# Kernel tuning notes

Measured on AMD Instinct MI355X. Metric: run time of the kernel, lower is better.

The kernel has to match this reference:

```python
import jax, jax.numpy as jnp
import numpy as np

B, C, HEADS, DH = 2, 1280, 20, 64
INNER = HEADS * DH
HW = 64
S = HW * HW
L = 77
ENC = 4096
GROUPS = 32
EPS = 1e-5
CREG = 1.0     # creg_ in __init__
NOATTN = 1.0   # global noattn
NORES = 1.0    # global noresidual


def setup_inputs() -> dict:
    key = jax.random.key(0)
    ks = jax.random.split(key, 10)
    std = 0.02
    return {
        "x": jax.random.normal(ks[0], (B, C, HW, HW), jnp.float32),
        "text": jax.random.normal(ks[1], (B, L, ENC), jnp.float32),
        "gn_gamma": jnp.ones((C,), jnp.float32),
        "gn_beta": jnp.zeros((C,), jnp.float32),
        "ln_gamma": jnp.ones((ENC,), jnp.float32),
        "ln_beta": jnp.zeros((ENC,), jnp.float32),
        "Wq": jax.random.normal(ks[2], (C, INNER), jnp.float32) * std,
        "bq": jnp.zeros((INNER,), jnp.float32),
        "Wk": jax.random.normal(ks[3], (ENC, INNER), jnp.float32) * std,
        "bk": jnp.zeros((INNER,), jnp.float32),
        "Wv": jax.random.normal(ks[4], (ENC, INNER), jnp.float32) * std,
        "bv": jnp.zeros((INNER,), jnp.float32),
        "Wo": jax.random.normal(ks[5], (INNER, C), jnp.float32) * std,
        "bo": jnp.zeros((C,), jnp.float32),
        "size_reg": jax.random.uniform(ks[6], (1, S, L), jnp.float32),
        "treg": jax.random.uniform(ks[7], (1,), jnp.float32),
        "mask": jax.random.randint(ks[8], (1, S, L), 0, 2, jnp.int32),
    }


def _group_norm(h, gamma, beta):
    # h: [B, C, S]; GroupNorm over (C//GROUPS, S) per group
    hg = h.reshape(B, GROUPS, -1)
    mu = hg.mean(-1, keepdims=True)
    var = hg.var(-1, keepdims=True)
    hn = ((hg - mu) * jax.lax.rsqrt(var + EPS)).reshape(B, C, S)
    return hn * gamma[None, :, None] + beta[None, :, None]


def _layer_norm(t, gamma, beta):
    mu = t.mean(-1, keepdims=True)
    var = t.var(-1, keepdims=True)
    return (t - mu) * jax.lax.rsqrt(var + EPS) * gamma + beta


def reference(x, text, gn_gamma, gn_beta, ln_gamma, ln_beta, Wq, bq, Wk, bk,
              Wv, bv, Wo, bo, size_reg, treg, mask):
    residual = x                              # [B, C, HW, HW]
    h = x.reshape(B, C, S)                    # spatial tokens
    h = _group_norm(h, gn_gamma, gn_beta).transpose(0, 2, 1)   # [B, S, C]
    enc = _layer_norm(text, ln_gamma, ln_beta)                  # [B, L, ENC]

    # head_to_batch_dim (out_dim=3): [B, T, inner] -> [B*heads, T, dh]
    q = (h @ Wq + bq).reshape(B, S, HEADS, DH).transpose(0, 2, 1, 3).reshape(B * HEADS, S, DH)
    k = (enc @ Wk + bk).reshape(B, L, HEADS, DH).transpose(0, 2, 1, 3).reshape(B * HEADS, L, DH)
    v = (enc @ Wv + bv).reshape(B, L, HEADS, DH).transpose(0, 2, 1, 3).reshape(B * HEADS, L, DH)

    scale = DH ** -0.5
    sim = jnp.einsum('bsd,bld->bsl', q, k) * scale            # [B*H, S, L]

    # region regularization applied only to the conditional (second) half
    half = (B * HEADS) // 2
    sim_u, sim_c = sim[:half], sim[half:]
    mn = sim_c.min(-1, keepdims=True)
    mx = sim_c.max(-1, keepdims=True)
    m = mask > 0                                               # [1, S, L] broadcasts over heads
    w = size_reg * CREG * treg[0]
    sim_c = sim_c + jnp.where(m, w, 0.0) * (mx - sim_c) - jnp.where(m, 0.0, w) * (sim_c - mn)
    sim = jnp.concatenate([sim_u, sim_c], axis=0)

    probs = jax.nn.softmax(sim, axis=-1)
    out = jnp.einsum('bsl,bld->bsd', probs, v)                 # [B*H, S, DH]
    # batch_to_head_dim: [B*H, S, DH] -> [B, S, inner]
    out = out.reshape(B, HEADS, S, DH).transpose(0, 2, 1, 3).reshape(B, S, INNER)
    out = out @ Wo + bo                                        # to_out[0]; dropout p=0
    out = out.transpose(0, 2, 1).reshape(residual.shape)       # [B, C, HW, HW]
    return out * NOATTN + residual * NORES
```

## Files before the change

### kernel.cpp

```cpp
#include <hip/hip_runtime.h>

typedef __bf16 bf16_t;
typedef __bf16 bf16x8 __attribute__((ext_vector_type(8)));
typedef float  f32x4  __attribute__((ext_vector_type(4)));
typedef unsigned int u32x4 __attribute__((ext_vector_type(4)));


__global__ __launch_bounds__(256) void k_transpose_cvt4(
    const float* __restrict__ w0, const float* __restrict__ w1,
    const float* __restrict__ w2, const float* __restrict__ w3,
    bf16_t* __restrict__ o0, bf16_t* __restrict__ o1,
    bf16_t* __restrict__ o2, bf16_t* __restrict__ o3)
{
  const int z = blockIdx.z;
  const float* in  = (z == 0) ? w0 : (z == 1) ? w1 : (z == 2) ? w2 : w3;
  bf16_t*      out = (z == 0) ? o0 : (z == 1) ? o1 : (z == 2) ? o2 : o3;
  const int R = (z < 2) ? 1280 : 4096;
  const int r0 = blockIdx.y * 64;
  if (r0 >= R) return;
  __shared__ float tile[64][33];
  const int c0 = blockIdx.x * 32;
  const int t = threadIdx.x;
#pragma unroll
  for (int it = 0; it < 8; ++it) {
    int r = it * 8 + (t >> 5), c = t & 31;
    tile[r][c] = in[(size_t)(r0 + r) * 1280 + c0 + c];
  }
  __syncthreads();
  {
    const int oc  = t >> 3;
    const int seg = t & 7;
    bf16x8 o;
#pragma unroll
    for (int e = 0; e < 8; ++e) o[e] = (bf16_t)tile[seg * 8 + e][oc];
    *(bf16x8*)(out + (size_t)(c0 + oc) * R + r0 + seg * 8) = o;
  }
}

__global__ __launch_bounds__(256) void k_gn_partial(
    const float* __restrict__ x, float* __restrict__ partial)
{
  const int bg    = blockIdx.x >> 5;
  const int chunk = blockIdx.x & 31;
  const float* p  = x + (size_t)bg * 163840 + (size_t)chunk * 5120;
  float s1 = 0.f, s2 = 0.f;
#pragma unroll
  for (int it = 0; it < 5; ++it) {
    float4 v = *(const float4*)(p + (size_t)(it * 256 + threadIdx.x) * 4);
    s1 += v.x + v.y + v.z + v.w;
    s2 += v.x * v.x + v.y * v.y + v.z * v.z + v.w * v.w;
  }
#pragma unroll
  for (int off = 32; off > 0; off >>= 1) {
    s1 += __shfl_down(s1, off);
    s2 += __shfl_down(s2, off);
  }
  __shared__ float r1[4], r2[4];
  if ((threadIdx.x & 63) == 0) { r1[threadIdx.x >> 6] = s1; r2[threadIdx.x >> 6] = s2; }
  __syncthreads();
  if (threadIdx.x == 0) {
    partial[blockIdx.x * 2]     = r1[0] + r1[1] + r1[2] + r1[3];
    partial[blockIdx.x * 2 + 1] = r2[0] + r2[1] + r2[2] + r2[3];
  }
}

__global__ __launch_bounds__(64) void k_gn_finalize(
    const float* __restrict__ partial, float* __restrict__ stats)
{
  const int bg = threadIdx.x;
  float t1 = 0.f, t2 = 0.f;
#pragma unroll
  for (int c = 0; c < 32; ++c) {
    t1 += partial[(bg * 32 + c) * 2];
    t2 += partial[(bg * 32 + c) * 2 + 1];
  }
  const float invN = 1.0f / 163840.0f;
  float mu  = t1 * invN;
  float var = t2 * invN - mu * mu;
  stats[bg * 2]     = mu;
  stats[bg * 2 + 1] = rsqrtf(var + 1e-5f);
}

__global__ __launch_bounds__(256) void k_gn_apply(
    const float* __restrict__ x, const float* __restrict__ stats,
    const float* __restrict__ gamma, const float* __restrict__ beta,
    bf16_t* __restrict__ h)
{
  __shared__ float tile[64][65];
  const int s0 = blockIdx.x * 64;
  const int c0 = blockIdx.y * 64;
  const int b  = blockIdx.z;
  const int t  = threadIdx.x;
#pragma unroll
  for (int it = 0; it < 16; ++it) {
    int cl = it * 4 + (t >> 6);
    int sl = t & 63;
    tile[cl][sl] = x[((size_t)(b * 1280 + c0 + cl) << 12) + s0 + sl];
  }
  __syncthreads();
#pragma unroll
  for (int it = 0; it < 2; ++it) {
    int i  = it * 256 + t;
    int sl = i >> 3;
    int cg = i & 7;
    bf16x8 o;
#pragma unroll
    for (int e = 0; e < 8; ++e) {
      int c  = c0 + cg * 8 + e;
      int g  = c / 40;
      float mu = stats[(b * 32 + g) * 2];
      float rs = stats[(b * 32 + g) * 2 + 1];
      o[e] = (bf16_t)((tile[cg * 8 + e][sl] - mu) * rs * gamma[c] + beta[c]);
    }
    *(bf16x8*)(h + (size_t)(b * 4096 + s0 + sl) * 1280 + c0 + cg * 8) = o;
  }
}

__global__ __launch_bounds__(256) void k_ln(
    const float* __restrict__ text, const float* __restrict__ g,
    const float* __restrict__ bta, bf16_t* __restrict__ enc)
{
  const int row = blockIdx.x;
  const float* p = text + (size_t)row * 4096;
  float s1 = 0.f, s2 = 0.f;
  for (int i = threadIdx.x; i < 1024; i += 256) {
    float4 v = *(const float4*)(p + (size_t)i * 4);
    s1 += v.x + v.y + v.z + v.w;
    s2 += v.x * v.x + v.y * v.y + v.z * v.z + v.w * v.w;
  }
#pragma unroll
  for (int off = 32; off > 0; off >>= 1) {
    s1 += __shfl_down(s1, off);
    s2 += __shfl_down(s2, off);
  }
  __shared__ float r1[4], r2[4], sh[2];
  if ((threadIdx.x & 63) == 0) { r1[threadIdx.x >> 6] = s1; r2[threadIdx.x >> 6] = s2; }
  __syncthreads();
  if (threadIdx.x == 0) {
    float t1 = r1[0] + r1[1] + r1[2] + r1[3];
    float t2 = r2[0] + r2[1] + r2[2] + r2[3];
    const float invN = 1.0f / 4096.0f;
    float mu  = t1 * invN;
    float var = t2 * invN - mu * mu;
    sh[0] = mu;
    sh[1] = rsqrtf(var + 1e-5f);
  }
  __syncthreads();
  const float mu = sh[0], rs = sh[1];
  for (int i = threadIdx.x; i < 1024; i += 256) {
    float4 v  = *(const float4*)(p + (size_t)i * 4);
    float4 gg = *(const float4*)(g + (size_t)i * 4);
    float4 bb = *(const float4*)(bta + (size_t)i * 4);
    bf16_t* o = enc + (size_t)row * 4096 + (size_t)i * 4;
    o[0] = (bf16_t)((v.x - mu) * rs * gg.x + bb.x);
    o[1] = (bf16_t)((v.y - mu) * rs * gg.y + bb.y);
    o[2] = (bf16_t)((v.z - mu) * rs * gg.z + bb.z);
    o[3] = (bf16_t)((v.w - mu) * rs * gg.w + bb.w);
  }
}

template <int EPI>
__global__ __launch_bounds__(256, 2) void k_gemm_big(
    const bf16_t* __restrict__ A, const bf16_t* __restrict__ BT,
    const float* __restrict__ bias, bf16_t* __restrict__ outb,
    const float* __restrict__ xres, float* __restrict__ dout,
    int lda, int klen, int nnt)
{
  __shared__ alignas(16) bf16_t smem[40960];
  const int tid  = threadIdx.x;
  const int lane = tid & 63;
  const int wv   = tid >> 6;

  const int cpx  = gridDim.x >> 3;
  const int nbid = (blockIdx.x & 7) * cpx + (blockIdx.x >> 3);
  const int mt   = nbid / nnt, ntile = nbid % nnt;
  const int m0   = mt * 256;
  const int n0   = ntile * 64;

  f32x4 acc[4][4];
  const f32x4 fz = {0.f, 0.f, 0.f, 0.f};
#pragma unroll
  for (int i = 0; i < 4; ++i)
#pragma unroll
    for (int j = 0; j < 4; ++j) acc[i][j] = fz;

  auto stage = [&](int buf, int kt) {
    bf16_t* sA = smem + buf * 16384;
    bf16_t* sB = smem + 32768 + buf * 4096;
#pragma unroll
    for (int it = 0; it < 8; ++it) {
      int slot = it * 256 + tid;
      int row  = slot >> 3, ch = slot & 7;
      const bf16_t* ga = A + (size_t)(m0 + row) * lda + kt + ((ch ^ (row & 7)) << 3);
      __builtin_amdgcn_global_load_lds(
          (const __attribute__((address_space(1))) void*)ga,
          (__attribute__((address_space(3))) void*)((char*)sA + slot * 16),
          16, 0, 0);
    }
#pragma unroll
    for (int it = 0; it < 2; ++it) {
      int slot = it * 256 + tid;
      int row  = slot >> 3, ch = slot & 7;
      const bf16_t* gb = BT + (size_t)(n0 + row) * lda + kt + ((ch ^ (row & 7)) << 3);
      __builtin_amdgcn_global_load_lds(
          (const __attribute__((address_space(1))) void*)gb,
          (__attribute__((address_space(3))) void*)((char*)sB + slot * 16),
          16, 0, 0);
    }
  };

  const int nt_k = klen >> 6;
  stage(0, 0);
  if (nt_k > 1) stage(1, 64);

  for (int t = 0; t < nt_k; ++t) {
    if (t + 1 < nt_k) { asm volatile("s_waitcnt vmcnt(10)" ::: "memory"); }
    else              { asm volatile("s_waitcnt vmcnt(0)" ::: "memory"); }
    __builtin_amdgcn_s_barrier();
    const char* pA = (const char*)(smem + (t & 1) * 16384);
    const char* pB = (const char*)(smem + 32768 + (t & 1) * 4096);
#pragma unroll
    for (int ks = 0; ks < 2; ++ks) {
      const int kb = ks * 64 + ((lane >> 4) << 4);
      bf16x8 af[4], bfg[4];
#pragma unroll
      for (int i = 0; i < 4; ++i) {
        int r = wv * 64 + i * 16 + (lane & 15);
        af[i] = *(const bf16x8*)(pA + r * 128 + (kb ^ ((r & 7) << 4)));
      }
#pragma unroll
      for (int j = 0; j < 4; ++j) {
        int c = j * 16 + (lane & 15);
        bfg[j] = *(const bf16x8*)(pB + c * 128 + (kb ^ ((c & 7) << 4)));
      }
#pragma unroll
      for (int i = 0; i < 4; ++i)
#pragma unroll
        for (int j = 0; j < 4; ++j)
          acc[i][j] = __builtin_amdgcn_mfma_f32_16x16x32_bf16(af[i], bfg[j], acc[i][j], 0, 0, 0);
    }
    asm volatile("s_waitcnt lgkmcnt(0)" ::: "memory");
    __builtin_amdgcn_s_barrier();
    if (t + 2 < nt_k) stage(t & 1, (t + 2) * 64);
  }

  if (EPI == 0) {
    bf16_t* cst = smem;
#pragma unroll
    for (int j = 0; j < 4; ++j) {
      const int n  = n0 + j * 16 + (lane & 15);
      const float bs = bias[n];
      const int cl = j * 16 + (lane & 15);
#pragma unroll
      for (int i = 0; i < 4; ++i) {
        const int rl = wv * 64 + i * 16 + ((lane >> 4) << 2);
#pragma unroll
        for (int r = 0; r < 4; ++r)
          cst[(rl + r) * 76 + cl] = (bf16_t)(acc[i][j][r] + bs);
      }
    }
    __syncthreads();
#pragma unroll
    for (int it = 0; it < 8; ++it) {
      int slot = it * 256 + tid;
      int row = slot >> 3, ch = slot & 7;
      u32x4 d = *(const u32x4*)(cst + row * 76 + ch * 8);
      *(u32x4*)(outb + (size_t)(m0 + row) * 1280 + n0 + ch * 8) = d;
    }
  } else {
#pragma unroll
    for (int i = 0; i < 4; ++i) {
      const int mrow = m0 + wv * 64 + i * 16 + ((lane >> 4) << 2);
#pragma unroll
      for (int j = 0; j < 4; ++j) {
        const int n = n0 + j * 16 + (lane & 15);
        const int b = mrow >> 12, s = mrow & 4095;
        const size_t off = ((size_t)(b * 1280 + n) << 12) + s;
        const float bs = bias[n];
        const float4 xr = *(const float4*)(xres + off);
        float4 o;
        o.x = acc[i][j][0] + bs + xr.x;
        o.y = acc[i][j][1] + bs + xr.y;
        o.z = acc[i][j][2] + bs + xr.z;
        o.w = acc[i][j][3] + bs + xr.w;
        *(float4*)(dout + off) = o;
      }
    }
  }
}

__global__ __launch_bounds__(256, 3) void k_gemm_kv(
    const bf16_t* __restrict__ A, const bf16_t* __restrict__ BT,
    float* __restrict__ outf, int M, int lda, int klen, int nnt, int nst)
{
  __shared__ alignas(16) bf16_t smem[24576];
  const int tid  = threadIdx.x;
  const int lane = tid & 63;
  const int wv   = tid >> 6;
  const int wm   = wv >> 1, wn = wv & 1;

  const int cpx  = gridDim.x >> 3;
  const int nbid = (blockIdx.x & 7) * cpx + (blockIdx.x >> 3);
  const int mt   = nbid / nnt, ntile = nbid % nnt;
  const int m0   = mt * 128;
  const int n0   = ntile * 64;
  const int kbeg = blockIdx.z * klen;

  f32x4 acc[4][2];
  const f32x4 fz = {0.f, 0.f, 0.f, 0.f};
#pragma unroll
  for (int i = 0; i < 4; ++i)
#pragma unroll
    for (int j = 0; j < 2; ++j) acc[i][j] = fz;

  auto stage = [&](int buf, int kt) {
    bf16_t* sA = smem + buf * 8192;
    bf16_t* sB = smem + 16384 + buf * 4096;
#pragma unroll
    for (int it = 0; it < 4; ++it) {
      int slot = it * 256 + tid;
      int row  = slot >> 3, ch = slot & 7;
      int grow = m0 + row; if (grow > M - 1) grow = M - 1;
      const bf16_t* ga = A + (size_t)grow * lda + kt + ((ch ^ (row & 7)) << 3);
      __builtin_amdgcn_global_load_lds(
          (const __attribute__((address_space(1))) void*)ga,
          (__attribute__((address_space(3))) void*)((char*)sA + slot * 16),
          16, 0, 0);
    }
#pragma unroll
    for (int it = 0; it < 2; ++it) {
      int slot = it * 256 + tid;
      int row  = slot >> 3, ch = slot & 7;
      const bf16_t* gb = BT + (size_t)(n0 + row) * lda + kt + ((ch ^ (row & 7)) << 3);
      __builtin_amdgcn_global_load_lds(
          (const __attribute__((address_space(1))) void*)gb,
          (__attribute__((address_space(3))) void*)((char*)sB + slot * 16),
          16, 0, 0);
    }
  };

  const int nt_k = klen >> 6;
  stage(0, kbeg);
  if (nt_k > 1) stage(1, kbeg + 64);

  for (int t = 0; t < nt_k; ++t) {
    if (t + 1 < nt_k) { asm volatile("s_waitcnt vmcnt(6)" ::: "memory"); }
    else              { asm volatile("s_waitcnt vmcnt(0)" ::: "memory"); }
    __builtin_amdgcn_s_barrier();
    const char* pA = (const char*)(smem + (t & 1) * 8192);
    const char* pB = (const char*)(smem + 16384 + (t & 1) * 4096);
#pragma unroll
    for (int ks = 0; ks < 2; ++ks) {
      const int kb = ks * 64 + ((lane >> 4) << 4);
      bf16x8 af[4], bfg[2];
#pragma unroll
      for (int i = 0; i < 4; ++i) {
        int r = wm * 64 + i * 16 + (lane & 15);
        af[i] = *(const bf16x8*)(pA + r * 128 + (kb ^ ((r & 7) << 4)));
      }
#pragma unroll
      for (int j = 0; j < 2; ++j) {
        int c = wn * 32 + j * 16 + (lane & 15);
        bfg[j] = *(const bf16x8*)(pB + c * 128 + (kb ^ ((c & 7) << 4)));
      }
#pragma unroll
      for (int i = 0; i < 4; ++i)
#pragma unroll
        for (int j = 0; j < 2; ++j)
          acc[i][j] = __builtin_amdgcn_mfma_f32_16x16x32_bf16(af[i], bfg[j], acc[i][j], 0, 0, 0);
    }
    asm volatile("s_waitcnt lgkmcnt(0)" ::: "memory");
    __builtin_amdgcn_s_barrier();
    if (t + 2 < nt_k) stage(t & 1, kbeg + (t + 2) * 64);
  }

#pragma unroll
  for (int i = 0; i < 4; ++i) {
    const int mrow = m0 + wm * 64 + i * 16 + ((lane >> 4) << 2);
#pragma unroll
    for (int j = 0; j < 2; ++j) {
      const int n = n0 + wn * 32 + j * 16 + (lane & 15);
#pragma unroll
      for (int r = 0; r < 4; ++r)
        if (mrow + r < M)
          outf[(size_t)blockIdx.z * 154 * nst + (size_t)(mrow + r) * nst + n] = acc[i][j][r];
    }
  }
}

__global__ __launch_bounds__(256) void k_kv_reduce(
    const float* __restrict__ part, const float* __restrict__ bk,
    const float* __restrict__ bv, bf16_t* __restrict__ kb, bf16_t* __restrict__ vb)
{
  const int idx = blockIdx.x * 256 + threadIdx.x;
  if (idx >= 154 * 2560) return;
  const int r = idx / 2560, n = idx % 2560;
  float s = (n < 1280) ? bk[n] : bv[n - 1280];
#pragma unroll
  for (int sp = 0; sp < 8; ++sp) s += part[(size_t)sp * (154 * 2560) + idx];
  if (n < 1280) kb[(size_t)r * 1280 + n] = (bf16_t)s;
  else          vb[(size_t)r * 1280 + n - 1280] = (bf16_t)s;
}

__global__ __launch_bounds__(256) void k_attn(
    const bf16_t* __restrict__ q, const bf16_t* __restrict__ kbuf,
    const bf16_t* __restrict__ vbuf, bf16_t* __restrict__ ao,
    const float* __restrict__ size_reg, const int* __restrict__ mask,
    const float* __restrict__ treg)
{
  __shared__ alignas(16) bf16_t sQ[64 * 64];
  __shared__ alignas(16) bf16_t sK[80 * 64];
  __shared__ alignas(16) bf16_t sVT[64 * 104];
  __shared__ alignas(16) bf16_t sP[4 * 16 * 104];
  const int s0   = blockIdx.x * 64;
  const int bh   = blockIdx.y;
  const int b    = bh / 20, head = bh % 20;
  const int tid  = threadIdx.x, lane = tid & 63, wv = tid >> 6;
  const int ntok = lane & 15;

  const u32x4 uz = {0u, 0u, 0u, 0u};
  for (int i = tid; i < 832; i += 256) ((u32x4*)sVT)[i] = uz;
  for (int i = tid; i < 832; i += 256) ((u32x4*)sP)[i]  = uz;

  const size_t qbase = ((size_t)(b * 4096 + s0)) * 1280 + head * 64;
  for (int slot = tid; slot < 512; slot += 256) {
    int row = slot >> 3, ch = slot & 7;
    u32x4 d = *(const u32x4*)(q + qbase + (size_t)row * 1280 + ((ch ^ (row & 7)) << 3));
    *(u32x4*)((char*)sQ + slot * 16) = d;
  }
  const size_t kvbase = ((size_t)(b * 77)) * 1280 + head * 64;
  for (int slot = tid; slot < 640; slot += 256) {
    int tok = slot >> 3, ch = slot & 7;
    u32x4 d = uz;
    if (tok < 77)
      d = *(const u32x4*)(kbuf + kvbase + (size_t)tok * 1280 + ((ch ^ (tok & 7)) << 3));
    *(u32x4*)((char*)sK + slot * 16) = d;
  }
  __syncthreads();
  for (int e = tid; e < 77 * 64; e += 256) {
    int tok = e >> 6, dh = e & 63;
    sVT[dh * 104 + tok] = vbuf[kvbase + (size_t)tok * 1280 + dh];
  }
  __syncthreads();

  f32x4 sim[5];
  const f32x4 fz = {0.f, 0.f, 0.f, 0.f};
#pragma unroll
  for (int nf = 0; nf < 5; ++nf) sim[nf] = fz;
  const int qrow = wv * 16 + (lane & 15);
#pragma unroll
  for (int ks = 0; ks < 2; ++ks) {
    const int kb = ks * 64 + ((lane >> 4) << 4);
    bf16x8 aq = *(const bf16x8*)((const char*)sQ + qrow * 128 + (kb ^ ((qrow & 7) << 4)));
#pragma unroll
    for (int nf = 0; nf < 5; ++nf) {
      int tok = nf * 16 + ntok;
      bf16x8 bk = *(const bf16x8*)((const char*)sK + tok * 128 + (kb ^ ((tok & 7) << 4)));
      sim[nf] = __builtin_amdgcn_mfma_f32_16x16x32_bf16(aq, bk, sim[nf], 0, 0, 0);
    }
  }

  float vv[5][4];
#pragma unroll
  for (int nf = 0; nf < 5; ++nf)
#pragma unroll
    for (int r = 0; r < 4; ++r) vv[nf][r] = sim[nf][r] * 0.125f;

  const int rbase = s0 + wv * 16 + ((lane >> 4) << 2);

  if (b == 1) {
    const float tr = treg[0];
#pragma unroll
    for (int r = 0; r < 4; ++r) {
      float mx = -1e30f, mn = 1e30f;
#pragma unroll
      for (int nf = 0; nf < 5; ++nf)
        if (nf * 16 + ntok < 77) { mx = fmaxf(mx, vv[nf][r]); mn = fminf(mn, vv[nf][r]); }
#pragma unroll
      for (int m = 1; m < 16; m <<= 1) {
        mx = fmaxf(mx, __shfl_xor(mx, m));
        mn = fminf(mn, __shfl_xor(mn, m));
      }
      const int srow = rbase + r;
#pragma unroll
      for (int nf = 0; nf < 5; ++nf) {
        int l = nf * 16 + ntok;
        if (l < 77) {
          float w  = size_reg[srow * 77 + l] * tr;
          int   mk = mask[srow * 77 + l];
          float v  = vv[nf][r];
          vv[nf][r] = (mk > 0) ? v + w * (mx - v) : v - w * (v - mn);
        }
      }
    }
  }

#pragma unroll
  for (int r = 0; r < 4; ++r) {
    float mx = -1e30f;
#pragma unroll
    for (int nf = 0; nf < 5; ++nf)
      if (nf * 16 + ntok < 77) mx = fmaxf(mx, vv[nf][r]);
#pragma unroll
    for (int m = 1; m < 16; m <<= 1) mx = fmaxf(mx, __shfl_xor(mx, m));
    float p[5]; float sm = 0.f;
#pragma unroll
    for (int nf = 0; nf < 5; ++nf) {
      bool val = (nf * 16 + ntok) < 77;
      p[nf] = val ? __expf(vv[nf][r] - mx) : 0.f;
      sm += p[nf];
    }
#pragma unroll
    for (int m = 1; m < 16; m <<= 1) sm += __shfl_xor(sm, m);
    const float inv = 1.0f / sm;
    const int prow = ((lane >> 4) << 2) + r;
#pragma unroll
    for (int nf = 0; nf < 5; ++nf)
      sP[wv * 1664 + prow * 104 + nf * 16 + ntok] = (bf16_t)(p[nf] * inv);
  }
  __syncthreads();

  f32x4 o[4];
#pragma unroll
  for (int fd = 0; fd < 4; ++fd) o[fd] = fz;
#pragma unroll
  for (int ks = 0; ks < 3; ++ks) {
    const int kb = ks * 64 + ((lane >> 4) << 4);
    bf16x8 ap = *(const bf16x8*)((const char*)sP + wv * 3328 + (lane & 15) * 208 + kb);
#pragma unroll
    for (int fd = 0; fd < 4; ++fd) {
      bf16x8 bv = *(const bf16x8*)((const char*)sVT + (fd * 16 + (lane & 15)) * 208 + kb);
      o[fd] = __builtin_amdgcn_mfma_f32_16x16x32_bf16(ap, bv, o[fd], 0, 0, 0);
    }
  }
  const size_t obase =
      ((size_t)(b * 4096 + s0 + wv * 16 + ((lane >> 4) << 2))) * 1280 + head * 64;
#pragma unroll
  for (int fd = 0; fd < 4; ++fd)
#pragma unroll
    for (int r = 0; r < 4; ++r)
      ao[obase + (size_t)r * 1280 + fd * 16 + (lane & 15)] = (bf16_t)o[fd][r];
}

extern "C" void kernel_launch(void* const* d_in, const int* in_sizes, int n_in,
                              void* d_out, int out_size, void* d_ws, size_t ws_size,
                              hipStream_t stream)
{
  const float* x    = (const float*)d_in[0];
  const float* text = (const float*)d_in[1];
  const float* gng  = (const float*)d_in[2];
  const float* gnb  = (const float*)d_in[3];
  const float* lng  = (const float*)d_in[4];
  const float* lnb  = (const float*)d_in[5];
  const float* Wq   = (const float*)d_in[6];
  const float* bq   = (const float*)d_in[7];
  const float* Wk   = (const float*)d_in[8];
  const float* bk   = (const float*)d_in[9];
  const float* Wv   = (const float*)d_in[10];
  const float* bv   = (const float*)d_in[11];
  const float* Wo   = (const float*)d_in[12];
  const float* bo   = (const float*)d_in[13];
  const float* sreg = (const float*)d_in[14];
  const float* treg = (const float*)d_in[15];
  const int*   msk  = (const int*)d_in[16];
  float* out = (float*)d_out;

  char* ws = (char*)d_ws;
  size_t off = 0;
  auto alloc = [&](size_t bytes) {
    char* p = ws + off;
    off += (bytes + 255) & ~(size_t)255;
    return p;
  };
  float*  partial = (float*)alloc(2048 * 2 * sizeof(float));
  float*  stats   = (float*)alloc(64 * 2 * sizeof(float));
  bf16_t* WqT = (bf16_t*)alloc((size_t)1280 * 1280 * 2);
  bf16_t* WkT = (bf16_t*)alloc((size_t)1280 * 4096 * 2);
  bf16_t* WvT = (bf16_t*)alloc((size_t)1280 * 4096 * 2);
  bf16_t* WoT = (bf16_t*)alloc((size_t)1280 * 1280 * 2);
  bf16_t* h   = (bf16_t*)alloc((size_t)8192 * 1280 * 2);
  bf16_t* enc = (bf16_t*)alloc((size_t)154 * 4096 * 2);
  bf16_t* qb  = (bf16_t*)alloc((size_t)8192 * 1280 * 2);
  bf16_t* kb  = (bf16_t*)alloc((size_t)154 * 1280 * 2);
  bf16_t* vb  = (bf16_t*)alloc((size_t)154 * 1280 * 2);
  float*  part = (float*)alloc((size_t)8 * 154 * 2560 * sizeof(float));

  k_transpose_cvt4<<<dim3(40, 64, 4), 256, 0, stream>>>(Wq, Wo, Wk, Wv,
                                                        WqT, WoT, WkT, WvT);

  k_gn_partial<<<2048, 256, 0, stream>>>(x, partial);
  k_gn_finalize<<<1, 64, 0, stream>>>(partial, stats);
  k_gn_apply<<<dim3(64, 20, 2), 256, 0, stream>>>(x, stats, gng, gnb, h);
  k_ln<<<154, 256, 0, stream>>>(text, lng, lnb, enc);

  k_gemm_big<0><<<dim3(640), 256, 0, stream>>>(h, WqT, bq, qb, nullptr, nullptr,
                                               1280, 1280, 20);
  k_gemm_kv<<<dim3(80, 1, 8), 256, 0, stream>>>(enc, WkT, part, 154, 4096, 512, 40, 2560);
  k_kv_reduce<<<1540, 256, 0, stream>>>(part, bk, bv, kb, vb);

  k_attn<<<dim3(64, 40), 256, 0, stream>>>(qb, kb, vb, h, sreg, msk, treg);

  k_gemm_big<2><<<dim3(640), 256, 0, stream>>>(h, WoT, bo, nullptr, x, out,
                                               1280, 1280, 20);
}
```

Measured before the change: 183.0 us.

## Shrink GEMM tile to 128x64 with 2x2 wave layout and triple-buffered LDS

```diff
diff --git a/kernel.cpp b/kernel.cpp
--- a/kernel.cpp
+++ b/kernel.cpp
@@ -160,100 +160,105 @@
 }
 
 template <int EPI>
-__global__ __launch_bounds__(256, 2) void k_gemm_big(
+__global__ __launch_bounds__(256, 2) void k_gemm(
     const bf16_t* __restrict__ A, const bf16_t* __restrict__ BT,
     const float* __restrict__ bias, bf16_t* __restrict__ outb,
     const float* __restrict__ xres, float* __restrict__ dout,
     int lda, int klen, int nnt)
 {
-  __shared__ alignas(16) bf16_t smem[40960];
+  __shared__ alignas(16) bf16_t smem[36864];
   const int tid  = threadIdx.x;
   const int lane = tid & 63;
   const int wv   = tid >> 6;
+  const int wm   = wv >> 1, wn = wv & 1;
 
   const int cpx  = gridDim.x >> 3;
   const int nbid = (blockIdx.x & 7) * cpx + (blockIdx.x >> 3);
   const int mt   = nbid / nnt, ntile = nbid % nnt;
-  const int m0   = mt * 256;
+  const int m0   = mt * 128;
   const int n0   = ntile * 64;
 
-  f32x4 acc[4][4];
+  f32x4 acc[4][2];
   const f32x4 fz = {0.f, 0.f, 0.f, 0.f};
 #pragma unroll
   for (int i = 0; i < 4; ++i)
 #pragma unroll
-    for (int j = 0; j < 4; ++j) acc[i][j] = fz;
-
-  auto stage = [&](int buf, int kt) {
-    bf16_t* sA = smem + buf * 16384;
-    bf16_t* sB = smem + 32768 + buf * 4096;
-#pragma unroll
-    for (int it = 0; it < 8; ++it) {
-      int slot = it * 256 + tid;
-      int row  = slot >> 3, ch = slot & 7;
+    for (int j = 0; j < 2; ++j) acc[i][j] = fz;
+
+  auto stage = [&](int slot, int kt) {
+    bf16_t* sA = smem + slot * 8192;
+    bf16_t* sB = smem + 24576 + slot * 4096;
+#pragma unroll
+    for (int it = 0; it < 4; ++it) {
+      int s = it * 256 + tid;
+      int row = s >> 3, ch = s & 7;
       const bf16_t* ga = A + (size_t)(m0 + row) * lda + kt + ((ch ^ (row & 7)) << 3);
       __builtin_amdgcn_global_load_lds(
           (const __attribute__((address_space(1))) void*)ga,
-          (__attribute__((address_space(3))) void*)((char*)sA + slot * 16),
+          (__attribute__((address_space(3))) void*)((char*)sA + s * 16),
           16, 0, 0);
     }
 #pragma unroll
     for (int it = 0; it < 2; ++it) {
-      int slot = it * 256 + tid;
-      int row  = slot >> 3, ch = slot & 7;
+      int s = it * 256 + tid;
+      int row = s >> 3, ch = s & 7;
       const bf16_t* gb = BT + (size_t)(n0 + row) * lda + kt + ((ch ^ (row & 7)) << 3);
       __builtin_amdgcn_global_load_lds(
           (const __attribute__((address_space(1))) void*)gb,
-          (__attribute__((address_space(3))) void*)((char*)sB + slot * 16),
+          (__attribute__((address_space(3))) void*)((char*)sB + s * 16),
           16, 0, 0);
     }
   };
 
   const int nt_k = klen >> 6;
   stage(0, 0);
-  if (nt_k > 1) stage(1, 64);
-
+  stage(1, 64);
+
+  int cur = 0, stg = 2;
   for (int t = 0; t < nt_k; ++t) {
-    if (t + 1 < nt_k) { asm volatile("s_waitcnt vmcnt(10)" ::: "memory"); }
+    if (t + 1 < nt_k) { asm volatile("s_waitcnt vmcnt(6)" ::: "memory"); }
     else              { asm volatile("s_waitcnt vmcnt(0)" ::: "memory"); }
     __builtin_amdgcn_s_barrier();
-    const char* pA = (const char*)(smem + (t & 1) * 16384);
-    const char* pB = (const char*)(smem + 32768 + (t & 1) * 4096);
+    if (t + 2 < nt_k) {
+      stage(stg, (t + 2) * 64);
+      stg = (stg == 2) ? 0 : stg + 1;
+    }
+    const char* pA = (const char*)(smem + cur * 8192);
+    const char* pB = (const char*)(smem + 24576 + cur * 4096);
 #pragma unroll
     for (int ks = 0; ks < 2; ++ks) {
       const int kb = ks * 64 + ((lane >> 4) << 4);
-      bf16x8 af[4], bfg[4];
+      bf16x8 af[4], bfg[2];
 #pragma unroll
       for (int i = 0; i < 4; ++i) {
-        int r = wv * 64 + i * 16 + (lane & 15);
+        int r = wm * 64 + i * 16 + (lane & 15);
         af[i] = *(const bf16x8*)(pA + r * 128 + (kb ^ ((r & 7) << 4)));
       }
 #pragma unroll
-      for (int j = 0; j < 4; ++j) {
-        int c = j * 16 + (lane & 15);
+      for (int j = 0; j < 2; ++j) {
+        int c = wn * 32 + j * 16 + (lane & 15);
         bfg[j] = *(const bf16x8*)(pB + c * 128 + (kb ^ ((c & 7) << 4)));
       }
 #pragma unroll
       for (int i = 0; i < 4; ++i)
 #pragma unroll
-        for (int j = 0; j < 4; ++j)
+        for (int j = 0; j < 2; ++j)
           acc[i][j] = __builtin_amdgcn_mfma_f32_16x16x32_bf16(af[i], bfg[j], acc[i][j], 0, 0, 0);
     }
-    asm volatile("s_waitcnt lgkmcnt(0)" ::: "memory");
-    __builtin_amdgcn_s_barrier();
-    if (t + 2 < nt_k) stage(t & 1, (t + 2) * 64);
-  }
+    cur = (cur == 2) ? 0 : cur + 1;
+  }
+  __syncthreads();
 
   if (EPI == 0) {
     bf16_t* cst = smem;
 #pragma unroll
-    for (int j = 0; j < 4; ++j) {
-      const int n  = n0 + j * 16 + (lane & 15);
+    for (int j = 0; j < 2; ++j) {
+      const int n  = n0 + wn * 32 + j * 16 + (lane & 15);
       const float bs = bias[n];
-      const int cl = j * 16 + (lane & 15);
+      const int cl = wn * 32 + j * 16 + (lane & 15);
 #pragma unroll
       for (int i = 0; i < 4; ++i) {
-        const int rl = wv * 64 + i * 16 + ((lane >> 4) << 2);
+        const int rl = wm * 64 + i * 16 + ((lane >> 4) << 2);
 #pragma unroll
         for (int r = 0; r < 4; ++r)
           cst[(rl + r) * 76 + cl] = (bf16_t)(acc[i][j][r] + bs);
@@ -261,7 +266,7 @@
     }
     __syncthreads();
 #pragma unroll
-    for (int it = 0; it < 8; ++it) {
+    for (int it = 0; it < 4; ++it) {
       int slot = it * 256 + tid;
       int row = slot >> 3, ch = slot & 7;
       u32x4 d = *(const u32x4*)(cst + row * 76 + ch * 8);
@@ -270,10 +275,10 @@
   } else {
 #pragma unroll
     for (int i = 0; i < 4; ++i) {
-      const int mrow = m0 + wv * 64 + i * 16 + ((lane >> 4) << 2);
-#pragma unroll
-      for (int j = 0; j < 4; ++j) {
-        const int n = n0 + j * 16 + (lane & 15);
+      const int mrow = m0 + wm * 64 + i * 16 + ((lane >> 4) << 2);
+#pragma unroll
+      for (int j = 0; j < 2; ++j) {
+        const int n = n0 + wn * 32 + j * 16 + (lane & 15);
         const int b = mrow >> 12, s = mrow & 4095;
         const size_t off = ((size_t)(b * 1280 + n) << 12) + s;
         const float bs = bias[n];
@@ -593,13 +598,13 @@
   k_gn_apply<<<dim3(64, 20, 2), 256, 0, stream>>>(x, stats, gng, gnb, h);
   k_ln<<<154, 256, 0, stream>>>(text, lng, lnb, enc);
 
-  k_gemm_big<0><<<dim3(640), 256, 0, stream>>>(h, WqT, bq, qb, nullptr, nullptr,
-                                               1280, 1280, 20);
+  k_gemm<0><<<dim3(1280), 256, 0, stream>>>(h, WqT, bq, qb, nullptr, nullptr,
+                                            1280, 1280, 20);
   k_gemm_kv<<<dim3(80, 1, 8), 256, 0, stream>>>(enc, WkT, part, 154, 4096, 512, 40, 2560);
   k_kv_reduce<<<1540, 256, 0, stream>>>(part, bk, bv, kb, vb);
 
   k_attn<<<dim3(64, 40), 256, 0, stream>>>(qb, kb, vb, h, sreg, msk, treg);
 
-  k_gemm_big<2><<<dim3(640), 256, 0, stream>>>(h, WoT, bo, nullptr, x, out,
-                                               1280, 1280, 20);
-}
+  k_gemm<2><<<dim3(1280), 256, 0, stream>>>(h, WoT, bo, nullptr, x, out,
+                                            1280, 1280, 20);
+}
```

Measured after the change: 177.5 us. 3.0% less time.
